# Kernel tuning notes

Hardware: AMD Instinct MI355X
Metric: run time of the kernel (lower is better)

The kernel has to match this reference:

```python
import jax, jax.numpy as jnp
import numpy as np

B, F, S, H1, O = 8192, 128, 128, 64, 1

def setup_inputs() -> dict:
    key = jax.random.key(0)
    ks = jax.random.split(key, 8)
    sc1 = 1.0  # Linear(1, S): torch init ~ U(-1,1); use scaled normals
    return {
        "x":  jax.random.normal(ks[0], (B, F), dtype=jnp.float32),
        "W1": jax.random.normal(ks[1], (F, S), dtype=jnp.float32) * sc1,
        "b1": jax.random.normal(ks[2], (F, S), dtype=jnp.float32) * 0.1,
        "W2": jax.random.normal(ks[3], (F, S, H1), dtype=jnp.float32) * (1.0 / np.sqrt(S)),
        "b2": jax.random.normal(ks[4], (F, H1), dtype=jnp.float32) * 0.1,
        "W3": jax.random.normal(ks[5], (F, H1, O), dtype=jnp.float32) * (1.0 / np.sqrt(H1)),
        "b3": jax.random.normal(ks[6], (F, O), dtype=jnp.float32) * 0.1,
        "bias": jnp.zeros((O,), dtype=jnp.float32),
    }

def reference(x, W1, b1, W2, b2, W3, b3, bias):
    # Per-feature net: Linear(1,S) -> ReLU -> Linear(S,H1) -> ReLU -> (Dropout=id at eval) -> Linear(H1,O)
    # Batched over the feature axis f (equivalent to the original Python loop + cat).
    h1 = jax.nn.relu(x[:, :, None] * W1[None, :, :] + b1[None, :, :])      # [B,F,S]
    h2 = jax.nn.relu(jnp.einsum('bfs,fsh->bfh', h1, W2) + b2[None, :, :])  # [B,F,H1]
    fo = jnp.einsum('bfh,fho->bfo', h2, W3) + b3[None, :, :]               # [B,F,O]
    # torch.cat(...,dim=1) of [B,1] slices -> [B,F]; sum(dim=1,keepdim=True)+bias -> [B,1]
    out = fo.reshape(B, F * O).sum(axis=1, keepdims=True) + bias           # [B,1]
    return out
```

## Files before the change

### kernel.cpp

```cpp
#include <hip/hip_runtime.h>
#include <hip/hip_bf16.h>

#define B_ 8192
#define F_ 128
#define S_ 128
#define H_ 64
#define NCHUNK 8

typedef __attribute__((ext_vector_type(4))) float f32x4;
typedef __attribute__((ext_vector_type(8))) short bf16x8;

static __device__ __forceinline__ short f2bf(float v) {
    __hip_bfloat16 t = __float2bfloat16(v);
    return __builtin_bit_cast(short, t);
}

__global__ __launch_bounds__(256) void nam_prologue(
    const float* __restrict__ bias, float* __restrict__ out,
    const float* __restrict__ W2,   bf16x8* __restrict__ W2bf,
    const float* __restrict__ x,    float* __restrict__ xT)
{
    __shared__ float t[32][33];
    const int blk = blockIdx.x;
    if (blk < 32) {
        int i = blk * 256 + threadIdx.x;
        out[i] = bias[0];
    } else if (blk < 544) {
        const int idx = (blk - 32) * 256 + threadIdx.x;
        const int l   = idx & 63;
        const int m   = (idx >> 6) & 3;
        const int kk  = (idx >> 8) & 3;
        const int f   = idx >> 10;
        const int l16 = l & 15, lg = l >> 4;
        const float* __restrict__ src =
            W2 + ((size_t)f * S_ + kk * 32 + lg * 8) * H_ + m * 16 + l16;
        bf16x8 v;
#pragma unroll
        for (int j = 0; j < 8; ++j) v[j] = f2bf(src[j * H_]);
        W2bf[idx] = v;
    } else {
        const int bid = blk - 544;
        const int li = threadIdx.x & 31;
        const int wi = threadIdx.x >> 5;
        const int b0 = (bid & 255) * 32;
        const int f0 = (bid >> 8) * 32;
#pragma unroll
        for (int r = wi; r < 32; r += 8)
            t[r][li] = x[(size_t)(b0 + r) * F_ + f0 + li];
        __syncthreads();
#pragma unroll
        for (int r = wi; r < 32; r += 8)
            xT[(size_t)(f0 + r) * B_ + b0 + li] = t[li][r];
    }
}

__global__ __launch_bounds__(256, 2) void nam_mfma(
    const float* __restrict__ xT,
    const float* __restrict__ W1,
    const float* __restrict__ b1,
    const bf16x8* __restrict__ W2bf,
    const float* __restrict__ b2,
    const float* __restrict__ W3,
    const float* __restrict__ b3,
    float* __restrict__ out)
{
    const int f     = blockIdx.x >> 3;
    const int chunk = blockIdx.x & 7;
    const int tid   = threadIdx.x;
    const int w     = tid >> 6;
    const int l     = tid & 63;
    const int l16   = l & 15;
    const int lg    = l >> 4;

    const int b0 = chunk * (B_ / NCHUNK) + w * 256;

    const bf16x8* __restrict__ W2f = W2bf + (size_t)f * 16 * 64 + l;
    bf16x8 afrag[16];
#pragma unroll
    for (int q = 0; q < 16; ++q) afrag[q] = W2f[q * 64];

    const float* __restrict__ W1f = W1 + f * S_;
    const float* __restrict__ b1f = b1 + f * S_;
    f32x4 w1r[8], b1r[8];
#pragma unroll
    for (int kk = 0; kk < 4; ++kk) {
        w1r[kk * 2]     = *(const f32x4*)(W1f + kk * 32 + lg * 8);
        w1r[kk * 2 + 1] = *(const f32x4*)(W1f + kk * 32 + lg * 8 + 4);
        b1r[kk * 2]     = *(const f32x4*)(b1f + kk * 32 + lg * 8);
        b1r[kk * 2 + 1] = *(const f32x4*)(b1f + kk * 32 + lg * 8 + 4);
    }

    const float* __restrict__ b2f = b2 + f * H_;
    const float* __restrict__ W3f = W3 + f * H_;
    f32x4 b2v[4], w3v[4];
#pragma unroll
    for (int m = 0; m < 4; ++m) {
        b2v[m] = *(const f32x4*)(b2f + m * 16 + lg * 4);
        w3v[m] = *(const f32x4*)(W3f + m * 16 + lg * 4);
    }
    const float b3f = b3[f];
    const float* __restrict__ xTf = xT + (size_t)f * B_;

    float xv0 = xTf[b0 + l16];
    float xv1 = xTf[b0 + 16 + l16];

#pragma unroll 1
    for (int it = 0; it < 8; ++it) {
        const int bbase = b0 + it * 32;
        float nx0 = 0.f, nx1 = 0.f;
        if (it < 7) {
            nx0 = xTf[bbase + 32 + l16];
            nx1 = xTf[bbase + 48 + l16];
        }

        f32x4 acc[4][2];
#pragma unroll
        for (int m = 0; m < 4; ++m) {
            acc[m][0] = (f32x4){0.f, 0.f, 0.f, 0.f};
            acc[m][1] = (f32x4){0.f, 0.f, 0.f, 0.f};
        }

#pragma unroll
        for (int kk = 0; kk < 4; ++kk) {
            bf16x8 bf0, bf1;
#pragma unroll
            for (int j = 0; j < 4; ++j) {
                bf0[j]     = f2bf(fmaxf(fmaf(xv0, w1r[kk*2][j],     b1r[kk*2][j]),     0.f));
                bf0[j + 4] = f2bf(fmaxf(fmaf(xv0, w1r[kk*2+1][j],   b1r[kk*2+1][j]),   0.f));
                bf1[j]     = f2bf(fmaxf(fmaf(xv1, w1r[kk*2][j],     b1r[kk*2][j]),     0.f));
                bf1[j + 4] = f2bf(fmaxf(fmaf(xv1, w1r[kk*2+1][j],   b1r[kk*2+1][j]),   0.f));
            }
#pragma unroll
            for (int m = 0; m < 4; ++m) {
                acc[m][0] = __builtin_amdgcn_mfma_f32_16x16x32_bf16(afrag[kk*4+m], bf0, acc[m][0], 0, 0, 0);
                acc[m][1] = __builtin_amdgcn_mfma_f32_16x16x32_bf16(afrag[kk*4+m], bf1, acc[m][1], 0, 0, 0);
            }
        }

        float fo0 = 0.f, fo1 = 0.f;
#pragma unroll
        for (int m = 0; m < 4; ++m) {
#pragma unroll
            for (int r = 0; r < 4; ++r) {
                fo0 = fmaf(fmaxf(acc[m][0][r] + b2v[m][r], 0.f), w3v[m][r], fo0);
                fo1 = fmaf(fmaxf(acc[m][1][r] + b2v[m][r], 0.f), w3v[m][r], fo1);
            }
        }
        fo0 += __shfl_xor(fo0, 16);
        fo0 += __shfl_xor(fo0, 32);
        fo1 += __shfl_xor(fo1, 16);
        fo1 += __shfl_xor(fo1, 32);
        if (lg == 0) {
            atomicAdd(&out[bbase + l16], fo0 + b3f);
            atomicAdd(&out[bbase + 16 + l16], fo1 + b3f);
        }
        xv0 = nx0;
        xv1 = nx1;
    }
}

extern "C" void kernel_launch(void* const* d_in, const int* in_sizes, int n_in,
                              void* d_out, int out_size, void* d_ws, size_t ws_size,
                              hipStream_t stream) {
    const float* x    = (const float*)d_in[0];
    const float* W1   = (const float*)d_in[1];
    const float* b1   = (const float*)d_in[2];
    const float* W2   = (const float*)d_in[3];
    const float* b2   = (const float*)d_in[4];
    const float* W3   = (const float*)d_in[5];
    const float* b3   = (const float*)d_in[6];
    const float* bias = (const float*)d_in[7];
    float* out = (float*)d_out;

    bf16x8* W2bf = (bf16x8*)d_ws;
    const size_t W2BF_BYTES = (size_t)F_ * 16 * 64 * 16;
    float* xT = (float*)((char*)d_ws + W2BF_BYTES);

    nam_prologue<<<32 + 512 + 1024, 256, 0, stream>>>(bias, out, W2, W2bf, x, xT);
    nam_mfma<<<F_ * NCHUNK, 256, 0, stream>>>(xT, W1, b1, W2bf, b2, W3, b3, out);
}
```

Measured before the change: 96.61 us.

## Drop prologue kernel, convert W2 in-kernel, replace atomics with partial-sum reduce

Removes the prologue kernel that pre-converted W2 to bf16 fragments, transposed x, and initialised the output. The main kernel now loads W2 in fp32 and converts it to bf16 per block, and reads x directly with a strided gather. Instead of atomically adding into the output, it writes per-feature partial sums to the workspace, and a new reduce kernel sums them over features and adds the bias. This trades atomic contention and a prologue pass for redundant W2 conversion (eight blocks per feature), uncoalesced x reads, and an extra 4 MB partial-sum round trip.

```diff
diff --git a/kernel.cpp b/kernel.cpp
--- a/kernel.cpp
+++ b/kernel.cpp
@@ -15,54 +15,15 @@
     return __builtin_bit_cast(short, t);
 }
 
-__global__ __launch_bounds__(256) void nam_prologue(
-    const float* __restrict__ bias, float* __restrict__ out,
-    const float* __restrict__ W2,   bf16x8* __restrict__ W2bf,
-    const float* __restrict__ x,    float* __restrict__ xT)
-{
-    __shared__ float t[32][33];
-    const int blk = blockIdx.x;
-    if (blk < 32) {
-        int i = blk * 256 + threadIdx.x;
-        out[i] = bias[0];
-    } else if (blk < 544) {
-        const int idx = (blk - 32) * 256 + threadIdx.x;
-        const int l   = idx & 63;
-        const int m   = (idx >> 6) & 3;
-        const int kk  = (idx >> 8) & 3;
-        const int f   = idx >> 10;
-        const int l16 = l & 15, lg = l >> 4;
-        const float* __restrict__ src =
-            W2 + ((size_t)f * S_ + kk * 32 + lg * 8) * H_ + m * 16 + l16;
-        bf16x8 v;
-#pragma unroll
-        for (int j = 0; j < 8; ++j) v[j] = f2bf(src[j * H_]);
-        W2bf[idx] = v;
-    } else {
-        const int bid = blk - 544;
-        const int li = threadIdx.x & 31;
-        const int wi = threadIdx.x >> 5;
-        const int b0 = (bid & 255) * 32;
-        const int f0 = (bid >> 8) * 32;
-#pragma unroll
-        for (int r = wi; r < 32; r += 8)
-            t[r][li] = x[(size_t)(b0 + r) * F_ + f0 + li];
-        __syncthreads();
-#pragma unroll
-        for (int r = wi; r < 32; r += 8)
-            xT[(size_t)(f0 + r) * B_ + b0 + li] = t[li][r];
-    }
-}
-
-__global__ __launch_bounds__(256, 2) void nam_mfma(
-    const float* __restrict__ xT,
+__global__ __launch_bounds__(256, 2) void nam_main(
+    const float* __restrict__ x,
     const float* __restrict__ W1,
     const float* __restrict__ b1,
-    const bf16x8* __restrict__ W2bf,
+    const float* __restrict__ W2,
     const float* __restrict__ b2,
     const float* __restrict__ W3,
     const float* __restrict__ b3,
-    float* __restrict__ out)
+    float* __restrict__ part)
 {
     const int f     = blockIdx.x >> 3;
     const int chunk = blockIdx.x & 7;
@@ -74,10 +35,20 @@
 
     const int b0 = chunk * (B_ / NCHUNK) + w * 256;
 
-    const bf16x8* __restrict__ W2f = W2bf + (size_t)f * 16 * 64 + l;
+    const float* __restrict__ W2f = W2 + (size_t)f * S_ * H_;
     bf16x8 afrag[16];
 #pragma unroll
-    for (int q = 0; q < 16; ++q) afrag[q] = W2f[q * 64];
+    for (int kk = 0; kk < 4; ++kk) {
+#pragma unroll
+        for (int m = 0; m < 4; ++m) {
+            const float* __restrict__ src =
+                W2f + (size_t)(kk * 32 + lg * 8) * H_ + m * 16 + l16;
+            bf16x8 v;
+#pragma unroll
+            for (int j = 0; j < 8; ++j) v[j] = f2bf(src[j * H_]);
+            afrag[kk * 4 + m] = v;
+        }
+    }
 
     const float* __restrict__ W1f = W1 + f * S_;
     const float* __restrict__ b1f = b1 + f * S_;
@@ -89,7 +60,6 @@
         b1r[kk * 2]     = *(const f32x4*)(b1f + kk * 32 + lg * 8);
         b1r[kk * 2 + 1] = *(const f32x4*)(b1f + kk * 32 + lg * 8 + 4);
     }
-
     const float* __restrict__ b2f = b2 + f * H_;
     const float* __restrict__ W3f = W3 + f * H_;
     f32x4 b2v[4], w3v[4];
@@ -99,18 +69,20 @@
         w3v[m] = *(const f32x4*)(W3f + m * 16 + lg * 4);
     }
     const float b3f = b3[f];
-    const float* __restrict__ xTf = xT + (size_t)f * B_;
 
-    float xv0 = xTf[b0 + l16];
-    float xv1 = xTf[b0 + 16 + l16];
+    const float* __restrict__ xb = x + f;
+    float* __restrict__ pf = part + (size_t)f * B_;
+
+    float xv0 = xb[(size_t)(b0 + l16) * F_];
+    float xv1 = xb[(size_t)(b0 + 16 + l16) * F_];
 
 #pragma unroll 1
     for (int it = 0; it < 8; ++it) {
         const int bbase = b0 + it * 32;
         float nx0 = 0.f, nx1 = 0.f;
         if (it < 7) {
-            nx0 = xTf[bbase + 32 + l16];
-            nx1 = xTf[bbase + 48 + l16];
+            nx0 = xb[(size_t)(bbase + 32 + l16) * F_];
+            nx1 = xb[(size_t)(bbase + 48 + l16) * F_];
         }
 
         f32x4 acc[4][2];
@@ -125,10 +97,10 @@
             bf16x8 bf0, bf1;
 #pragma unroll
             for (int j = 0; j < 4; ++j) {
-                bf0[j]     = f2bf(fmaxf(fmaf(xv0, w1r[kk*2][j],     b1r[kk*2][j]),     0.f));
-                bf0[j + 4] = f2bf(fmaxf(fmaf(xv0, w1r[kk*2+1][j],   b1r[kk*2+1][j]),   0.f));
-                bf1[j]     = f2bf(fmaxf(fmaf(xv1, w1r[kk*2][j],     b1r[kk*2][j]),     0.f));
-                bf1[j + 4] = f2bf(fmaxf(fmaf(xv1, w1r[kk*2+1][j],   b1r[kk*2+1][j]),   0.f));
+                bf0[j]     = f2bf(fmaxf(fmaf(xv0, w1r[kk*2][j],   b1r[kk*2][j]),   0.f));
+                bf0[j + 4] = f2bf(fmaxf(fmaf(xv0, w1r[kk*2+1][j], b1r[kk*2+1][j]), 0.f));
+                bf1[j]     = f2bf(fmaxf(fmaf(xv1, w1r[kk*2][j],   b1r[kk*2][j]),   0.f));
+                bf1[j + 4] = f2bf(fmaxf(fmaf(xv1, w1r[kk*2+1][j], b1r[kk*2+1][j]), 0.f));
             }
 #pragma unroll
             for (int m = 0; m < 4; ++m) {
@@ -151,12 +123,27 @@
         fo1 += __shfl_xor(fo1, 16);
         fo1 += __shfl_xor(fo1, 32);
         if (lg == 0) {
-            atomicAdd(&out[bbase + l16], fo0 + b3f);
-            atomicAdd(&out[bbase + 16 + l16], fo1 + b3f);
+            pf[bbase + l16]      = fo0 + b3f;
+            pf[bbase + 16 + l16] = fo1 + b3f;
         }
         xv0 = nx0;
         xv1 = nx1;
     }
+}
+
+__global__ __launch_bounds__(256) void nam_reduce(const float* __restrict__ part,
+                                                  const float* __restrict__ bias,
+                                                  float* __restrict__ out) {
+    const int b = blockIdx.x * 256 + threadIdx.x;
+    float s0 = 0.f, s1 = 0.f, s2 = 0.f, s3 = 0.f;
+#pragma unroll 8
+    for (int f = 0; f < F_; f += 4) {
+        s0 += part[(size_t)f * B_ + b];
+        s1 += part[(size_t)(f + 1) * B_ + b];
+        s2 += part[(size_t)(f + 2) * B_ + b];
+        s3 += part[(size_t)(f + 3) * B_ + b];
+    }
+    out[b] = (s0 + s1) + (s2 + s3) + bias[0];
 }
 
 extern "C" void kernel_launch(void* const* d_in, const int* in_sizes, int n_in,
@@ -170,12 +157,9 @@
     const float* W3   = (const float*)d_in[5];
     const float* b3   = (const float*)d_in[6];
     const float* bias = (const float*)d_in[7];
-    float* out = (float*)d_out;
+    float* out  = (float*)d_out;
+    float* part = (float*)d_ws;
 
-    bf16x8* W2bf = (bf16x8*)d_ws;
-    const size_t W2BF_BYTES = (size_t)F_ * 16 * 64 * 16;
-    float* xT = (float*)((char*)d_ws + W2BF_BYTES);
-
-    nam_prologue<<<32 + 512 + 1024, 256, 0, stream>>>(bias, out, W2, W2bf, x, xT);
-    nam_mfma<<<F_ * NCHUNK, 256, 0, stream>>>(xT, W1, b1, W2bf, b2, W3, b3, out);
+    nam_main<<<F_ * NCHUNK, 256, 0, stream>>>(x, W1, b1, W2, b2, W3, b3, part);
+    nam_reduce<<<B_ / 256, 256, 0, stream>>>(part, bias, out);
 }
```

Measured after the change: 104.9 us. 8.6% more time.
